# Performance work log

Hardware: AMD Instinct MI355X
Metric: run time of the kernel (lower is better)

The kernel has to match this reference:

```python
import jax, jax.numpy as jnp
import numpy as np

T, B, XIN, H, A = 4096, 1024, 2, 16, 4


def setup_inputs() -> dict:
    key = jax.random.key(0)
    ks = jax.random.split(key, 16)
    inp = {
        "x": jax.random.normal(ks[0], (T * B, XIN), dtype=jnp.float32),
        "done": jax.random.randint(ks[1], (T * B,), 0, 2, dtype=jnp.int32),
        "action": jax.random.randint(ks[2], (T * B,), 0, A, dtype=jnp.int32),
        "h0": jax.random.normal(ks[3], (B, H), dtype=jnp.float32) * 0.1,
        "c0": jax.random.normal(ks[4], (B, H), dtype=jnp.float32) * 0.1,
        # MLP: Linear(XIN, 16) (orthogonal init approximated by scaled normal)
        "w1": jax.random.normal(ks[5], (H, XIN), dtype=jnp.float32) * (1.0 / np.sqrt(XIN)),
        "b1": jnp.zeros((H,), dtype=jnp.float32),
        # LSTM(16, 16): gate order i, f, g, o (PyTorch convention)
        "w_ih": jax.random.normal(ks[6], (4 * H, H), dtype=jnp.float32) * (1.0 / np.sqrt(H)),
        "w_hh": jax.random.normal(ks[7], (4 * H, H), dtype=jnp.float32) * (1.0 / np.sqrt(H)),
        "b_ih": jnp.zeros((4 * H,), dtype=jnp.float32),
        "b_hh": jnp.zeros((4 * H,), dtype=jnp.float32),
        "actor_w": jax.random.normal(ks[8], (A, H), dtype=jnp.float32) * 0.01,
        "actor_b": jnp.zeros((A,), dtype=jnp.float32),
        "critic_w": jax.random.normal(ks[9], (1, H), dtype=jnp.float32) * (1.0 / np.sqrt(H)),
        "critic_b": jnp.zeros((1,), dtype=jnp.float32),
    }
    return inp


def reference(x, done, action, h0, c0, w1, b1, w_ih, w_hh, b_ih, b_hh,
              actor_w, actor_b, critic_w, critic_b):
    # MLP encoder: Linear(XIN,16) + ReLU, then reshape to [T, B, 16]
    hid = jax.nn.relu(x @ w1.T + b1)
    hid = hid.reshape(-1, h0.shape[0], H)          # [T, B, H]
    done_f = done.reshape(-1, h0.shape[0]).astype(hid.dtype)  # [T, B]

    def step(carry, inp):
        h, c = carry
        xt, dt = inp
        m = (1.0 - dt)[:, None]                    # reset mask per env
        h = h * m
        c = c * m
        gates = xt @ w_ih.T + b_ih + h @ w_hh.T + b_hh   # [B, 4H]
        i, f, g, o = jnp.split(gates, 4, axis=-1)
        i = jax.nn.sigmoid(i)
        f = jax.nn.sigmoid(f)
        g = jnp.tanh(g)
        o = jax.nn.sigmoid(o)
        c = f * c + i * g
        h = o * jnp.tanh(c)
        return (h, c), h

    (hN, cN), hs = jax.lax.scan(step, (h0, c0), (hid, done_f))
    hidden = hs.reshape(-1, H)                     # [T*B, H]

    logits = hidden @ actor_w.T + actor_b          # [T*B, A]
    logp_all = jax.nn.log_softmax(logits, axis=-1)
    logp = jnp.take_along_axis(logp_all, action[:, None].astype(jnp.int32), axis=1)[:, 0]
    entropy = -jnp.sum(jnp.exp(logp_all) * logp_all, axis=-1)
    value = (hidden @ critic_w.T + critic_b)[:, 0]
    return action, logp, entropy, value, hN, cN
```

## Files before the change

kernel.cpp:

```cpp
#include <hip/hip_runtime.h>

#define TT 4096
#define BB 1024
#define LCH 5
#define CH 32
#define NC 128
#define TB 4194304
#define OFF_LOGP (TB)
#define OFF_ENT  (2*TB)
#define OFF_VAL  (3*TB)
#define OFF_HN   (4*TB)
#define OFF_CN   (4*TB + 16384)

typedef float    f32x2 __attribute__((ext_vector_type(2)));
typedef float    f32x4 __attribute__((ext_vector_type(4)));
typedef _Float16 f16x4 __attribute__((ext_vector_type(4)));

__device__ __forceinline__ float fsig(float x){
    return __builtin_amdgcn_rcpf(1.f + __expf(-x));
}
__device__ __forceinline__ float ftanh_(float x){
    return 1.f - 2.f*__builtin_amdgcn_rcpf(1.f + __expf(2.f*x));
}
__device__ __forceinline__ f16x4 to_h4(f32x4 v){
    f16x4 r;
    r[0]=(_Float16)v[0]; r[1]=(_Float16)v[1]; r[2]=(_Float16)v[2]; r[3]=(_Float16)v[3];
    return r;
}
__device__ __forceinline__ f32x4 from_h4(f16x4 v){
    f32x4 r;
    r[0]=(float)v[0]; r[1]=(float)v[1]; r[2]=(float)v[2]; r[3]=(float)v[3];
    return r;
}
__device__ __forceinline__ f32x4 mfma16(f16x4 a, f16x4 b, f32x4 c){
    return __builtin_amdgcn_mfma_f32_16x16x16f16(a, b, c, 0, 0, 0);
}

#define KPARAMS const float* __restrict__ x, const int* __restrict__ done, \
    const int* __restrict__ action, const float* __restrict__ h0, \
    const float* __restrict__ c0, const float* __restrict__ w1, \
    const float* __restrict__ b1, const float* __restrict__ w_ih, \
    const float* __restrict__ w_hh, const float* __restrict__ bsum, \
    const float* __restrict__ hw16, \
    const float* __restrict__ actor_w, const float* __restrict__ actor_b, \
    const float* __restrict__ critic_w, const float* __restrict__ critic_b, \
    float* __restrict__ out, float* __restrict__ carry, int* __restrict__ valid

#define KARGS x,done,action,h0,c0,w1,b1,w_ih,w_hh,bsum,hw16,actor_w,actor_b,critic_w,critic_b,out,carry,valid

struct Frags {
    f16x4 wih[4], whh[4], hw;
    f32x4 biasC[4], biasH;
    f32x2 w1r[4];
    f32x4 b1r;
};

__device__ __forceinline__ void load_frags(Frags& F, int lo, int hi,
    const float* w1, const float* b1, const float* w_ih, const float* w_hh,
    const float* bsum, const float* hw16, const float* actor_b,
    const float* critic_b)
{
#pragma unroll
    for (int mt = 0; mt < 4; mt++) {
        F.wih[mt]   = to_h4(*(const f32x4*)(w_ih + (16*mt+lo)*16 + 4*hi));
        F.whh[mt]   = to_h4(*(const f32x4*)(w_hh + (16*mt+lo)*16 + 4*hi));
        F.biasC[mt] = *(const f32x4*)(bsum + 16*mt + 4*hi);
    }
    F.hw = to_h4(*(const f32x4*)(hw16 + lo*16 + 4*hi));
    if (hi == 0)       F.biasH = *(const f32x4*)(actor_b);
    else if (hi == 1)  F.biasH = (f32x4){critic_b[0], 0.f, 0.f, 0.f};
    else               F.biasH = (f32x4){0.f, 0.f, 0.f, 0.f};
#pragma unroll
    for (int r = 0; r < 4; r++) {
        F.w1r[r] = *(const f32x2*)(w1 + (4*hi+r)*2);
        F.b1r[r] = b1[4*hi+r];
    }
}

__device__ __forceinline__ void step_mfma(const Frags& F, f16x4& hh, f32x4& cc,
    f32x2 xv, int a, int idx, bool do_store, int hi, float* __restrict__ out)
{
    f32x4 hid;
#pragma unroll
    for (int r = 0; r < 4; r++)
        hid[r] = fmaxf(fmaf(F.w1r[r][0], xv[0], fmaf(F.w1r[r][1], xv[1], F.b1r[r])), 0.f);
    f16x4 hidh = to_h4(hid);
    f32x4 g0 = mfma16(F.whh[0], hh, F.biasC[0]);
    f32x4 g1 = mfma16(F.whh[1], hh, F.biasC[1]);
    f32x4 g2 = mfma16(F.whh[2], hh, F.biasC[2]);
    f32x4 g3 = mfma16(F.whh[3], hh, F.biasC[3]);
    g0 = mfma16(F.wih[0], hidh, g0);
    g1 = mfma16(F.wih[1], hidh, g1);
    g2 = mfma16(F.wih[2], hidh, g2);
    g3 = mfma16(F.wih[3], hidh, g3);
    f32x4 hn;
#pragma unroll
    for (int r = 0; r < 4; r++) {
        float si = fsig(g0[r]), sf = fsig(g1[r]);
        float sg = ftanh_(g2[r]), so = fsig(g3[r]);
        float cv = fmaf(sf, cc[r], si*sg);
        cc[r] = cv;
        hn[r] = so * ftanh_(cv);
    }
    hh = to_h4(hn);
    f32x4 dh = mfma16(F.hw, hh, F.biasH);
    if (do_store) {
        if (hi == 0) {
            float e0 = __expf(dh[0]), e1 = __expf(dh[1]);
            float e2 = __expf(dh[2]), e3 = __expf(dh[3]);
            float s  = e0+e1+e2+e3;
            float ls = __logf(s);
            float t  = e0*dh[0] + e1*dh[1] + e2*dh[2] + e3*dh[3];
            float ent = ls - t*__builtin_amdgcn_rcpf(s);
            float lsel = (a==0) ? dh[0] : (a==1) ? dh[1] : (a==2) ? dh[2] : dh[3];
            out[idx]            = (float)a;
            out[OFF_LOGP + idx] = lsel - ls;
            out[OFF_ENT  + idx] = ent;
        } else if (hi == 1) {
            out[OFF_VAL + idx] = dh[0];
        }
    }
}

__global__ __launch_bounds__(256, 4) void k_phase1(KPARAMS)
{
    const int tid  = blockIdx.x*256 + threadIdx.x;
    const int lane = tid & 63;
    const int lo = lane & 15, hi = lane >> 4;
    const int w    = tid >> 6;
    const int ch   = w >> 6;
    const int base = (w & 63) << 4;
    const int b    = base + lo;
    const int t0   = ch << LCH;

    Frags F;
    load_frags(F, lo, hi, w1, b1, w_ih, w_hh, bsum, hw16, actor_b, critic_b);

    f16x4 hh = {(_Float16)0.f,(_Float16)0.f,(_Float16)0.f,(_Float16)0.f};
    f32x4 cc = {0.f,0.f,0.f,0.f};
    int hr = 0;

    int   d_cur = done[t0*BB + b];
    f32x2 x_cur = *(const f32x2*)(x + 2*(size_t)(t0*BB + b));
    int   a_cur = action[t0*BB + b];

#pragma unroll 2
    for (int s = 0; s < CH; s++) {
        const int idx = (t0 + s)*BB + b;
        const int   d  = d_cur;
        const f32x2 xv = x_cur;
        const int   a  = a_cur;
        if (s + 1 < CH) {
            d_cur = done[idx + BB];
            x_cur = *(const f32x2*)(x + 2*(size_t)(idx + BB));
            a_cur = action[idx + BB];
        }
        hr |= d;
        if (d) {
            hh = (f16x4){(_Float16)0.f,(_Float16)0.f,(_Float16)0.f,(_Float16)0.f};
            cc = (f32x4){0.f,0.f,0.f,0.f};
        }
        step_mfma(F, hh, cc, xv, a, idx, true, hi, out);
    }
    if (hr) {
        f32x4 hf = from_h4(hh);
#pragma unroll
        for (int r = 0; r < 4; r++) {
            carry[(ch*32 + 4*hi + r)*BB + b]      = hf[r];
            carry[(ch*32 + 16 + 4*hi + r)*BB + b] = cc[r];
        }
    }
    if (hi == 0) valid[ch*BB + b] = hr;
}

__global__ __launch_bounds__(256, 4) void k_phase2(KPARAMS)
{
    const int tid  = blockIdx.x*256 + threadIdx.x;
    const int lane = tid & 63;
    const int lo = lane & 15, hi = lane >> 4;
    const int w    = tid >> 6;
    const int ch   = w >> 6;
    const int base = (w & 63) << 4;
    const int b    = base + lo;
    const int t0   = ch << LCH;

    Frags F;
    load_frags(F, lo, hi, w1, b1, w_ih, w_hh, bsum, hw16, actor_b, critic_b);

    f32x4 hf, cc;
    bool active;
    if (ch == 0) {
        hf = *(const f32x4*)(h0 + b*16 + 4*hi);
        cc = *(const f32x4*)(c0 + b*16 + 4*hi);
        active = true;
    } else {
        active = (valid[(ch-1)*BB + b] != 0);
#pragma unroll
        for (int r = 0; r < 4; r++) {
            hf[r] = carry[((ch-1)*32 + 4*hi + r)*BB + b];
            cc[r] = carry[((ch-1)*32 + 16 + 4*hi + r)*BB + b];
        }
    }
    f16x4 hh = to_h4(hf);

    for (int s = 0; s < CH; s++) {
        if (!__ballot(active)) break;
        const int idx = (t0 + s)*BB + b;
        const int d = done[idx];
        if (d) active = false;
        const f32x2 xv = *(const f32x2*)(x + 2*(size_t)idx);
        const int a = action[idx];
        step_mfma(F, hh, cc, xv, a, idx, active, hi, out);
    }

    if (ch == NC-1) {
        if (active) {
            f32x4 ho = from_h4(hh);
#pragma unroll
            for (int r = 0; r < 4; r++) {
                out[OFF_HN + b*16 + 4*hi + r] = ho[r];
                out[OFF_CN + b*16 + 4*hi + r] = cc[r];
            }
        } else if (valid[(NC-1)*BB + b]) {
#pragma unroll
            for (int r = 0; r < 4; r++) {
                out[OFF_HN + b*16 + 4*hi + r] = carry[((NC-1)*32 + 4*hi + r)*BB + b];
                out[OFF_CN + b*16 + 4*hi + r] = carry[((NC-1)*32 + 16 + 4*hi + r)*BB + b];
            }
        }
    }
}

__device__ void cell_scalar(const float* x, const int* action,
    const float* w1, const float* b1, const float* w_ih, const float* w_hh,
    const float* bsum, const float* actor_w, const float* actor_b,
    const float* critic_w, const float* critic_b, float* out,
    int t, int b, float h[16], float c[16])
{
    const int idx = t*BB + b;
    float x0 = x[2*(size_t)idx], x1 = x[2*(size_t)idx+1];
    float hid[16];
#pragma unroll
    for (int k = 0; k < 16; k++)
        hid[k] = fmaxf(fmaf(w1[2*k], x0, fmaf(w1[2*k+1], x1, b1[k])), 0.f);
    float nh[16], nc[16];
#pragma unroll
    for (int k = 0; k < 16; k++) {
        float ai = bsum[k], af = bsum[16+k], ag = bsum[32+k], ao = bsum[48+k];
#pragma unroll
        for (int j = 0; j < 16; j++) {
            ai = fmaf(w_ih[k*16+j],      hid[j], ai);
            af = fmaf(w_ih[(16+k)*16+j], hid[j], af);
            ag = fmaf(w_ih[(32+k)*16+j], hid[j], ag);
            ao = fmaf(w_ih[(48+k)*16+j], hid[j], ao);
        }
#pragma unroll
        for (int j = 0; j < 16; j++) {
            ai = fmaf(w_hh[k*16+j],      h[j], ai);
            af = fmaf(w_hh[(16+k)*16+j], h[j], af);
            ag = fmaf(w_hh[(32+k)*16+j], h[j], ag);
            ao = fmaf(w_hh[(48+k)*16+j], h[j], ao);
        }
        float si = fsig(ai), sf = fsig(af), sg = ftanh_(ag), so = fsig(ao);
        float cv = fmaf(sf, c[k], si*sg);
        nc[k] = cv; nh[k] = so*ftanh_(cv);
    }
#pragma unroll
    for (int k = 0; k < 16; k++) { h[k] = nh[k]; c[k] = nc[k]; }
    float l0=actor_b[0], l1=actor_b[1], l2=actor_b[2], l3=actor_b[3], v=critic_b[0];
#pragma unroll
    for (int j = 0; j < 16; j++) {
        l0 = fmaf(actor_w[j],    h[j], l0);
        l1 = fmaf(actor_w[16+j], h[j], l1);
        l2 = fmaf(actor_w[32+j], h[j], l2);
        l3 = fmaf(actor_w[48+j], h[j], l3);
        v  = fmaf(critic_w[j],   h[j], v);
    }
    float mx = fmaxf(fmaxf(l0,l1), fmaxf(l2,l3));
    float e0=__expf(l0-mx), e1=__expf(l1-mx), e2=__expf(l2-mx), e3=__expf(l3-mx);
    float s = e0+e1+e2+e3, ls = __logf(s), inv = __builtin_amdgcn_rcpf(s);
    float lp0=l0-mx-ls, lp1=l1-mx-ls, lp2=l2-mx-ls, lp3=l3-mx-ls;
    int a = action[idx];
    float lp = (a==0)?lp0:(a==1)?lp1:(a==2)?lp2:lp3;
    out[idx]            = (float)a;
    out[OFF_LOGP + idx] = lp;
    out[OFF_ENT  + idx] = -(e0*lp0+e1*lp1+e2*lp2+e3*lp3)*inv;
    out[OFF_VAL  + idx] = v;
}

__global__ void k_phase3(KPARAMS)
{
    int b = blockIdx.x*blockDim.x + threadIdx.x;
    if (b >= BB) return;
    bool anybad = false;
    for (int ch = 0; ch < NC; ch++) anybad |= (valid[ch*BB + b] == 0);
    if (!anybad) return;

    int fixed_until = 0;
    for (int ch = 0; ch < NC; ch++) {
        if (valid[ch*BB + b]) continue;
        int t0 = ch << LCH;
        if (t0 < fixed_until) continue;
        float h[16], c[16];
        if (ch == 0) {
#pragma unroll
            for (int k = 0; k < 16; k++) { h[k] = h0[b*16+k]; c[k] = c0[b*16+k]; }
        } else {
#pragma unroll
            for (int k = 0; k < 16; k++) {
                h[k] = carry[((ch-1)*32 + k)*BB + b];
                c[k] = carry[((ch-1)*32 + 16 + k)*BB + b];
            }
        }
        int t;
        for (t = t0; t < TT; t++) {
            if (done[t*BB + b]) break;
            cell_scalar(x, action, w1, b1, w_ih, w_hh, bsum,
                        actor_w, actor_b, critic_w, critic_b, out, t, b, h, c);
            if (((t+1) & (CH-1)) == 0) {
                int cc2 = t >> LCH;
#pragma unroll
                for (int k = 0; k < 16; k++) {
                    carry[(cc2*32 + k)*BB + b]      = h[k];
                    carry[(cc2*32 + 16 + k)*BB + b] = c[k];
                }
                valid[cc2*BB + b] = 1;
            }
        }
        if (t == TT) {
#pragma unroll
            for (int k = 0; k < 16; k++) {
                out[OFF_HN + b*16 + k] = h[k];
                out[OFF_CN + b*16 + k] = c[k];
            }
        }
        fixed_until = t;
    }
    if (valid[(NC-1)*BB + b]) {
#pragma unroll
        for (int k = 0; k < 16; k++) {
            out[OFF_HN + b*16 + k] = carry[((NC-1)*32 + k)*BB + b];
            out[OFF_CN + b*16 + k] = carry[((NC-1)*32 + 16 + k)*BB + b];
        }
    }
}

__global__ void k_prep(const float* __restrict__ b_ih, const float* __restrict__ b_hh,
                       const float* __restrict__ actor_w, const float* __restrict__ critic_w,
                       float* __restrict__ bsum, float* __restrict__ hw16)
{
    int i = threadIdx.x;
    if (i < 64) bsum[i] = b_ih[i] + b_hh[i];
    int row = i >> 4, k = i & 15;
    float v = 0.f;
    if (row < 4)        v = actor_w[row*16 + k];
    else if (row == 4)  v = critic_w[k];
    hw16[i] = v;
}

extern "C" void kernel_launch(void* const* d_in, const int* in_sizes, int n_in,
                              void* d_out, int out_size, void* d_ws, size_t ws_size,
                              hipStream_t stream)
{
    const float* x        = (const float*)d_in[0];
    const int*   done     = (const int*)  d_in[1];
    const int*   action   = (const int*)  d_in[2];
    const float* h0       = (const float*)d_in[3];
    const float* c0       = (const float*)d_in[4];
    const float* w1       = (const float*)d_in[5];
    const float* b1       = (const float*)d_in[6];
    const float* w_ih     = (const float*)d_in[7];
    const float* w_hh     = (const float*)d_in[8];
    const float* b_ih     = (const float*)d_in[9];
    const float* b_hh     = (const float*)d_in[10];
    const float* actor_w  = (const float*)d_in[11];
    const float* actor_b  = (const float*)d_in[12];
    const float* critic_w = (const float*)d_in[13];
    const float* critic_b = (const float*)d_in[14];
    float* out = (float*)d_out;

    float* bsum  = (float*)d_ws;
    float* hw16  = (float*)((char*)d_ws + 256);
    float* carry = (float*)((char*)d_ws + 2048);
    int*   valid = (int*)((char*)d_ws + 2048 + (size_t)NC*32*BB*4);

    hipLaunchKernelGGL(k_prep, dim3(1), dim3(256), 0, stream,
                       b_ih, b_hh, actor_w, critic_w, bsum, hw16);

    const int nthreads = NC*(BB/16)*64;
    hipLaunchKernelGGL(k_phase1, dim3(nthreads/256), dim3(256), 0, stream, KARGS);
    hipLaunchKernelGGL(k_phase2, dim3(nthreads/256), dim3(256), 0, stream, KARGS);
    hipLaunchKernelGGL(k_phase3, dim3(BB/256), dim3(256), 0, stream, KARGS);
}
```

Baseline: 164.5 us.

## Use rational tanh for LSTM gates and interleave two batch tiles per wave

Sigmoid gates are rewritten as 0.5*tanh(x/2)+0.5. The one-half scaling is folded into pre-scaled W_ih, W_hh and bias copies made in the prep kernel. All gate nonlinearities then use a clamped Padé rational tanh approximation (one rcp per element instead of exp+rcp). Each wave now handles two 16-env tiles, interleaving two independent recurrent chains to hide MFMA and transcendental latency, which halves the grid. The Padé approximation adds error for large arguments, and the changed reset masking and doubled register use may cut occupancy.

```diff
diff --git a/kernel.cpp b/kernel.cpp
--- a/kernel.cpp
+++ b/kernel.cpp
@@ -16,12 +16,28 @@
 typedef float    f32x4 __attribute__((ext_vector_type(4)));
 typedef _Float16 f16x4 __attribute__((ext_vector_type(4)));
 
+__device__ __forceinline__ f32x4 splat4(float v){ return (f32x4){v,v,v,v}; }
+
 __device__ __forceinline__ float fsig(float x){
     return __builtin_amdgcn_rcpf(1.f + __expf(-x));
 }
 __device__ __forceinline__ float ftanh_(float x){
     return 1.f - 2.f*__builtin_amdgcn_rcpf(1.f + __expf(2.f*x));
 }
+
+__device__ __forceinline__ f32x4 ptanh4(f32x4 x){
+    f32x4 x2 = x*x;
+    f32x4 x4 = x2*x2;
+    f32x4 nu = x * (__builtin_elementwise_fma(x2, splat4(105.f), splat4(945.f)) + x4);
+    f32x4 de = __builtin_elementwise_fma(x4, splat4(15.f),
+               __builtin_elementwise_fma(x2, splat4(420.f), splat4(945.f)));
+    f32x4 q;
+#pragma unroll
+    for (int i = 0; i < 4; i++)
+        q[i] = __builtin_amdgcn_fmed3f(nu[i]*__builtin_amdgcn_rcpf(de[i]), -1.f, 1.f);
+    return q;
+}
+
 __device__ __forceinline__ f16x4 to_h4(f32x4 v){
     f16x4 r;
     r[0]=(_Float16)v[0]; r[1]=(_Float16)v[1]; r[2]=(_Float16)v[2]; r[3]=(_Float16)v[3];
@@ -41,12 +57,13 @@
     const float* __restrict__ c0, const float* __restrict__ w1, \
     const float* __restrict__ b1, const float* __restrict__ w_ih, \
     const float* __restrict__ w_hh, const float* __restrict__ bsum, \
-    const float* __restrict__ hw16, \
+    const float* __restrict__ bsum_s, const float* __restrict__ wih_s, \
+    const float* __restrict__ whh_s, const float* __restrict__ hw16, \
     const float* __restrict__ actor_w, const float* __restrict__ actor_b, \
     const float* __restrict__ critic_w, const float* __restrict__ critic_b, \
     float* __restrict__ out, float* __restrict__ carry, int* __restrict__ valid
 
-#define KARGS x,done,action,h0,c0,w1,b1,w_ih,w_hh,bsum,hw16,actor_w,actor_b,critic_w,critic_b,out,carry,valid
+#define KARGS x,done,action,h0,c0,w1,b1,w_ih,w_hh,bsum,bsum_s,wih_s,whh_s,hw16,actor_w,actor_b,critic_w,critic_b,out,carry,valid
 
 struct Frags {
     f16x4 wih[4], whh[4], hw;
@@ -56,20 +73,20 @@
 };
 
 __device__ __forceinline__ void load_frags(Frags& F, int lo, int hi,
-    const float* w1, const float* b1, const float* w_ih, const float* w_hh,
-    const float* bsum, const float* hw16, const float* actor_b,
+    const float* w1, const float* b1, const float* wih_s, const float* whh_s,
+    const float* bsum_s, const float* hw16, const float* actor_b,
     const float* critic_b)
 {
 #pragma unroll
     for (int mt = 0; mt < 4; mt++) {
-        F.wih[mt]   = to_h4(*(const f32x4*)(w_ih + (16*mt+lo)*16 + 4*hi));
-        F.whh[mt]   = to_h4(*(const f32x4*)(w_hh + (16*mt+lo)*16 + 4*hi));
-        F.biasC[mt] = *(const f32x4*)(bsum + 16*mt + 4*hi);
+        F.wih[mt]   = to_h4(*(const f32x4*)(wih_s + (16*mt+lo)*16 + 4*hi));
+        F.whh[mt]   = to_h4(*(const f32x4*)(whh_s + (16*mt+lo)*16 + 4*hi));
+        F.biasC[mt] = *(const f32x4*)(bsum_s + 16*mt + 4*hi);
     }
     F.hw = to_h4(*(const f32x4*)(hw16 + lo*16 + 4*hi));
     if (hi == 0)       F.biasH = *(const f32x4*)(actor_b);
     else if (hi == 1)  F.biasH = (f32x4){critic_b[0], 0.f, 0.f, 0.f};
-    else               F.biasH = (f32x4){0.f, 0.f, 0.f, 0.f};
+    else               F.biasH = splat4(0.f);
 #pragma unroll
     for (int r = 0; r < 4; r++) {
         F.w1r[r] = *(const f32x2*)(w1 + (4*hi+r)*2);
@@ -93,25 +110,25 @@
     g1 = mfma16(F.wih[1], hidh, g1);
     g2 = mfma16(F.wih[2], hidh, g2);
     g3 = mfma16(F.wih[3], hidh, g3);
-    f32x4 hn;
-#pragma unroll
-    for (int r = 0; r < 4; r++) {
-        float si = fsig(g0[r]), sf = fsig(g1[r]);
-        float sg = ftanh_(g2[r]), so = fsig(g3[r]);
-        float cv = fmaf(sf, cc[r], si*sg);
-        cc[r] = cv;
-        hn[r] = so * ftanh_(cv);
-    }
+    f32x4 ti = ptanh4(g0);
+    f32x4 tf = ptanh4(g1);
+    f32x4 tg = ptanh4(g2);
+    f32x4 to_ = ptanh4(g3);
+    f32x4 i_ = __builtin_elementwise_fma(ti, splat4(0.5f), splat4(0.5f));
+    f32x4 f_ = __builtin_elementwise_fma(tf, splat4(0.5f), splat4(0.5f));
+    f32x4 o_ = __builtin_elementwise_fma(to_, splat4(0.5f), splat4(0.5f));
+    cc = __builtin_elementwise_fma(f_, cc, i_*tg);
+    f32x4 hn = o_ * ptanh4(cc);
     hh = to_h4(hn);
     f32x4 dh = mfma16(F.hw, hh, F.biasH);
     if (do_store) {
         if (hi == 0) {
             float e0 = __expf(dh[0]), e1 = __expf(dh[1]);
             float e2 = __expf(dh[2]), e3 = __expf(dh[3]);
-            float s  = e0+e1+e2+e3;
-            float ls = __logf(s);
-            float t  = e0*dh[0] + e1*dh[1] + e2*dh[2] + e3*dh[3];
-            float ent = ls - t*__builtin_amdgcn_rcpf(s);
+            float sE = e0+e1+e2+e3;
+            float ls = __logf(sE);
+            float tE = e0*dh[0] + e1*dh[1] + e2*dh[2] + e3*dh[3];
+            float ent = ls - tE*__builtin_amdgcn_rcpf(sE);
             float lsel = (a==0) ? dh[0] : (a==1) ? dh[1] : (a==2) ? dh[2] : dh[3];
             out[idx]            = (float)a;
             out[OFF_LOGP + idx] = lsel - ls;
@@ -128,49 +145,60 @@
     const int lane = tid & 63;
     const int lo = lane & 15, hi = lane >> 4;
     const int w    = tid >> 6;
-    const int ch   = w >> 6;
-    const int base = (w & 63) << 4;
-    const int b    = base + lo;
+    const int ch   = w >> 5;
+    const int base = (w & 31) << 5;
+    const int bA   = base + lo, bB = bA + 16;
     const int t0   = ch << LCH;
 
     Frags F;
-    load_frags(F, lo, hi, w1, b1, w_ih, w_hh, bsum, hw16, actor_b, critic_b);
-
-    f16x4 hh = {(_Float16)0.f,(_Float16)0.f,(_Float16)0.f,(_Float16)0.f};
-    f32x4 cc = {0.f,0.f,0.f,0.f};
-    int hr = 0;
-
-    int   d_cur = done[t0*BB + b];
-    f32x2 x_cur = *(const f32x2*)(x + 2*(size_t)(t0*BB + b));
-    int   a_cur = action[t0*BB + b];
-
-#pragma unroll 2
+    load_frags(F, lo, hi, w1, b1, wih_s, whh_s, bsum_s, hw16, actor_b, critic_b);
+
+    const f16x4 hz = {(_Float16)0.f,(_Float16)0.f,(_Float16)0.f,(_Float16)0.f};
+    f16x4 hhA = hz, hhB = hz;
+    f32x4 ccA = splat4(0.f), ccB = splat4(0.f);
+    int hrA = 0, hrB = 0;
+
+    int   dA = done[t0*BB + bA], dB = done[t0*BB + bB];
+    f32x2 xA = *(const f32x2*)(x + 2*(size_t)(t0*BB + bA));
+    f32x2 xB = *(const f32x2*)(x + 2*(size_t)(t0*BB + bB));
+    int   aA = action[t0*BB + bA], aB = action[t0*BB + bB];
+
+#pragma unroll 1
     for (int s = 0; s < CH; s++) {
-        const int idx = (t0 + s)*BB + b;
-        const int   d  = d_cur;
-        const f32x2 xv = x_cur;
-        const int   a  = a_cur;
+        const int idxA = (t0+s)*BB + bA, idxB = idxA + 16;
+        const int ddA = dA, ddB = dB, aaA = aA, aaB = aB;
+        const f32x2 xxA = xA, xxB = xB;
         if (s + 1 < CH) {
-            d_cur = done[idx + BB];
-            x_cur = *(const f32x2*)(x + 2*(size_t)(idx + BB));
-            a_cur = action[idx + BB];
-        }
-        hr |= d;
-        if (d) {
-            hh = (f16x4){(_Float16)0.f,(_Float16)0.f,(_Float16)0.f,(_Float16)0.f};
-            cc = (f32x4){0.f,0.f,0.f,0.f};
-        }
-        step_mfma(F, hh, cc, xv, a, idx, true, hi, out);
-    }
-    if (hr) {
-        f32x4 hf = from_h4(hh);
+            dA = done[idxA + BB];            dB = done[idxB + BB];
+            xA = *(const f32x2*)(x + 2*(size_t)(idxA + BB));
+            xB = *(const f32x2*)(x + 2*(size_t)(idxB + BB));
+            aA = action[idxA + BB];          aB = action[idxB + BB];
+        }
+        hrA |= ddA; hrB |= ddB;
+        const float mA = ddA ? 0.f : 1.f, mB = ddB ? 0.f : 1.f;
+        hhA *= (_Float16)mA; ccA *= mA;
+        hhB *= (_Float16)mB; ccB *= mB;
+        step_mfma(F, hhA, ccA, xxA, aaA, idxA, true, hi, out);
+        step_mfma(F, hhB, ccB, xxB, aaB, idxB, true, hi, out);
+    }
+    if (hrA) {
+        f32x4 hf = from_h4(hhA);
 #pragma unroll
         for (int r = 0; r < 4; r++) {
-            carry[(ch*32 + 4*hi + r)*BB + b]      = hf[r];
-            carry[(ch*32 + 16 + 4*hi + r)*BB + b] = cc[r];
-        }
-    }
-    if (hi == 0) valid[ch*BB + b] = hr;
+            carry[(ch*32 + 4*hi + r)*BB + bA]      = hf[r];
+            carry[(ch*32 + 16 + 4*hi + r)*BB + bA] = ccA[r];
+        }
+    }
+    if (hrB) {
+        f32x4 hf = from_h4(hhB);
+#pragma unroll
+        for (int r = 0; r < 4; r++) {
+            carry[(ch*32 + 4*hi + r)*BB + bB]      = hf[r];
+            carry[(ch*32 + 16 + 4*hi + r)*BB + bB] = ccB[r];
+        }
+    }
+    if (hi == 0)      valid[ch*BB + bA] = hrA;
+    else if (hi == 1) valid[ch*BB + bB] = hrB;
 }
 
 __global__ __launch_bounds__(256, 4) void k_phase2(KPARAMS)
@@ -179,53 +207,76 @@
     const int lane = tid & 63;
     const int lo = lane & 15, hi = lane >> 4;
     const int w    = tid >> 6;
-    const int ch   = w >> 6;
-    const int base = (w & 63) << 4;
-    const int b    = base + lo;
+    const int ch   = w >> 5;
+    const int base = (w & 31) << 5;
+    const int bA   = base + lo, bB = bA + 16;
     const int t0   = ch << LCH;
 
     Frags F;
-    load_frags(F, lo, hi, w1, b1, w_ih, w_hh, bsum, hw16, actor_b, critic_b);
-
-    f32x4 hf, cc;
-    bool active;
+    load_frags(F, lo, hi, w1, b1, wih_s, whh_s, bsum_s, hw16, actor_b, critic_b);
+
+    f32x4 hfA, cfA, hfB, cfB;
+    bool actA, actB;
     if (ch == 0) {
-        hf = *(const f32x4*)(h0 + b*16 + 4*hi);
-        cc = *(const f32x4*)(c0 + b*16 + 4*hi);
-        active = true;
+        hfA = *(const f32x4*)(h0 + bA*16 + 4*hi);
+        cfA = *(const f32x4*)(c0 + bA*16 + 4*hi);
+        hfB = *(const f32x4*)(h0 + bB*16 + 4*hi);
+        cfB = *(const f32x4*)(c0 + bB*16 + 4*hi);
+        actA = actB = true;
     } else {
-        active = (valid[(ch-1)*BB + b] != 0);
+        actA = valid[(ch-1)*BB + bA] != 0;
+        actB = valid[(ch-1)*BB + bB] != 0;
 #pragma unroll
         for (int r = 0; r < 4; r++) {
-            hf[r] = carry[((ch-1)*32 + 4*hi + r)*BB + b];
-            cc[r] = carry[((ch-1)*32 + 16 + 4*hi + r)*BB + b];
-        }
-    }
-    f16x4 hh = to_h4(hf);
+            hfA[r] = carry[((ch-1)*32 + 4*hi + r)*BB + bA];
+            cfA[r] = carry[((ch-1)*32 + 16 + 4*hi + r)*BB + bA];
+            hfB[r] = carry[((ch-1)*32 + 4*hi + r)*BB + bB];
+            cfB[r] = carry[((ch-1)*32 + 16 + 4*hi + r)*BB + bB];
+        }
+    }
+    f16x4 hhA = to_h4(hfA), hhB = to_h4(hfB);
+    f32x4 ccA = cfA, ccB = cfB;
 
     for (int s = 0; s < CH; s++) {
-        if (!__ballot(active)) break;
-        const int idx = (t0 + s)*BB + b;
-        const int d = done[idx];
-        if (d) active = false;
-        const f32x2 xv = *(const f32x2*)(x + 2*(size_t)idx);
-        const int a = action[idx];
-        step_mfma(F, hh, cc, xv, a, idx, active, hi, out);
+        if (!__ballot(actA | actB)) break;
+        const int idxA = (t0+s)*BB + bA, idxB = idxA + 16;
+        const int ddA = done[idxA], ddB = done[idxB];
+        if (ddA) actA = false;
+        if (ddB) actB = false;
+        const f32x2 xxA = *(const f32x2*)(x + 2*(size_t)idxA);
+        const f32x2 xxB = *(const f32x2*)(x + 2*(size_t)idxB);
+        const int aaA = action[idxA], aaB = action[idxB];
+        step_mfma(F, hhA, ccA, xxA, aaA, idxA, actA, hi, out);
+        step_mfma(F, hhB, ccB, xxB, aaB, idxB, actB, hi, out);
     }
 
     if (ch == NC-1) {
-        if (active) {
-            f32x4 ho = from_h4(hh);
+        if (actA) {
+            f32x4 ho = from_h4(hhA);
 #pragma unroll
             for (int r = 0; r < 4; r++) {
-                out[OFF_HN + b*16 + 4*hi + r] = ho[r];
-                out[OFF_CN + b*16 + 4*hi + r] = cc[r];
-            }
-        } else if (valid[(NC-1)*BB + b]) {
+                out[OFF_HN + bA*16 + 4*hi + r] = ho[r];
+                out[OFF_CN + bA*16 + 4*hi + r] = ccA[r];
+            }
+        } else if (valid[(NC-1)*BB + bA]) {
 #pragma unroll
             for (int r = 0; r < 4; r++) {
-                out[OFF_HN + b*16 + 4*hi + r] = carry[((NC-1)*32 + 4*hi + r)*BB + b];
-                out[OFF_CN + b*16 + 4*hi + r] = carry[((NC-1)*32 + 16 + 4*hi + r)*BB + b];
+                out[OFF_HN + bA*16 + 4*hi + r] = carry[((NC-1)*32 + 4*hi + r)*BB + bA];
+                out[OFF_CN + bA*16 + 4*hi + r] = carry[((NC-1)*32 + 16 + 4*hi + r)*BB + bA];
+            }
+        }
+        if (actB) {
+            f32x4 ho = from_h4(hhB);
+#pragma unroll
+            for (int r = 0; r < 4; r++) {
+                out[OFF_HN + bB*16 + 4*hi + r] = ho[r];
+                out[OFF_CN + bB*16 + 4*hi + r] = ccB[r];
+            }
+        } else if (valid[(NC-1)*BB + bB]) {
+#pragma unroll
+            for (int r = 0; r < 4; r++) {
+                out[OFF_HN + bB*16 + 4*hi + r] = carry[((NC-1)*32 + 4*hi + r)*BB + bB];
+                out[OFF_CN + bB*16 + 4*hi + r] = carry[((NC-1)*32 + 16 + 4*hi + r)*BB + bB];
             }
         }
     }
@@ -346,16 +397,32 @@
 }
 
 __global__ void k_prep(const float* __restrict__ b_ih, const float* __restrict__ b_hh,
+                       const float* __restrict__ w_ih, const float* __restrict__ w_hh,
                        const float* __restrict__ actor_w, const float* __restrict__ critic_w,
-                       float* __restrict__ bsum, float* __restrict__ hw16)
+                       float* __restrict__ bsum, float* __restrict__ bsum_s,
+                       float* __restrict__ hw16, float* __restrict__ wih_s,
+                       float* __restrict__ whh_s)
 {
     int i = threadIdx.x;
-    if (i < 64) bsum[i] = b_ih[i] + b_hh[i];
-    int row = i >> 4, k = i & 15;
-    float v = 0.f;
-    if (row < 4)        v = actor_w[row*16 + k];
-    else if (row == 4)  v = critic_w[k];
-    hw16[i] = v;
+    if (i < 64) {
+        float s = b_ih[i] + b_hh[i];
+        bsum[i] = s;
+        bool sg = (i < 32) || (i >= 48);
+        bsum_s[i] = sg ? 0.5f*s : s;
+    }
+    {
+        int row = i >> 4, k = i & 15;
+        float v = 0.f;
+        if (row < 4)        v = actor_w[row*16 + k];
+        else if (row == 4)  v = critic_w[k];
+        hw16[i] = v;
+    }
+    for (int j = i; j < 1024; j += 256) {
+        int row = j >> 4;
+        float sc = ((row < 32) || (row >= 48)) ? 0.5f : 1.f;
+        wih_s[j] = sc * w_ih[j];
+        whh_s[j] = sc * w_hh[j];
+    }
 }
 
 extern "C" void kernel_launch(void* const* d_in, const int* in_sizes, int n_in,
@@ -379,15 +446,19 @@
     const float* critic_b = (const float*)d_in[14];
     float* out = (float*)d_out;
 
-    float* bsum  = (float*)d_ws;
-    float* hw16  = (float*)((char*)d_ws + 256);
-    float* carry = (float*)((char*)d_ws + 2048);
-    int*   valid = (int*)((char*)d_ws + 2048 + (size_t)NC*32*BB*4);
+    float* bsum   = (float*)d_ws;
+    float* bsum_s = (float*)((char*)d_ws + 256);
+    float* hw16   = (float*)((char*)d_ws + 512);
+    float* wih_s  = (float*)((char*)d_ws + 1536);
+    float* whh_s  = (float*)((char*)d_ws + 5632);
+    float* carry  = (float*)((char*)d_ws + 16384);
+    int*   valid  = (int*)((char*)d_ws + 16384 + (size_t)NC*32*BB*4);
 
     hipLaunchKernelGGL(k_prep, dim3(1), dim3(256), 0, stream,
-                       b_ih, b_hh, actor_w, critic_w, bsum, hw16);
-
-    const int nthreads = NC*(BB/16)*64;
+                       b_ih, b_hh, w_ih, w_hh, actor_w, critic_w,
+                       bsum, bsum_s, hw16, wih_s, whh_s);
+
+    const int nthreads = NC*(BB/32)*64;
     hipLaunchKernelGGL(k_phase1, dim3(nthreads/256), dim3(256), 0, stream, KARGS);
     hipLaunchKernelGGL(k_phase2, dim3(nthreads/256), dim3(256), 0, stream, KARGS);
     hipLaunchKernelGGL(k_phase3, dim3(BB/256), dim3(256), 0, stream, KARGS);
```

Result: slower. 199.5 us (+21.3%).
